# Optimization experiments

Measured on AMD Instinct MI355X. Metric: run time of the kernel, lower is better.

## Reference

```python
import jax, jax.numpy as jnp
import numpy as np

EMBED_DIM = 768
NUM_HEADS = 12
FF_DIM = 3072
HEAD_DIM = EMBED_DIM // NUM_HEADS
LN_EPS = 1e-5


def setup_inputs() -> dict:
    key = jax.random.key(0)
    ks = jax.random.split(key, 10)
    C, F = EMBED_DIM, FF_DIM
    s = lambda d: 1.0 / np.sqrt(d)
    return {
        "x": jax.random.normal(ks[0], (2, 2048, C), dtype=jnp.float32),
        "w_qkv": jax.random.normal(ks[1], (C, 3 * C), dtype=jnp.float32) * s(C),
        "w_out": jax.random.normal(ks[2], (C, C), dtype=jnp.float32) * s(C),
        "ln1_g": jnp.ones((C,), jnp.float32),
        "ln1_b": jnp.zeros((C,), jnp.float32),
        "ln2_g": jnp.ones((C,), jnp.float32),
        "ln2_b": jnp.zeros((C,), jnp.float32),
        "w1": jax.random.normal(ks[3], (C, F), dtype=jnp.float32) * s(C),
        "b1": jnp.zeros((F,), jnp.float32),
        "w2": jax.random.normal(ks[4], (F, C), dtype=jnp.float32) * s(F),
        "b2": jnp.zeros((C,), jnp.float32),
    }


def _layernorm(x, g, b):
    mu = jnp.mean(x, axis=-1, keepdims=True)
    var = jnp.var(x, axis=-1, keepdims=True)
    return (x - mu) * jax.lax.rsqrt(var + LN_EPS) * g + b


def _attention(x, w_qkv, w_out):
    B, T, C = x.shape
    qkv = x @ w_qkv                               # [B,T,3C]
    q, k, v = jnp.split(qkv, 3, axis=2)
    def heads(t):  # [B,T,C] -> [B,H,T,Dh]
        return t.reshape(B, T, NUM_HEADS, HEAD_DIM).transpose(0, 2, 1, 3)
    q, k, v = heads(q), heads(k), heads(v)
    att = jnp.einsum("bhqd,bhkd->bhqk", q, k) / np.sqrt(HEAD_DIM)
    mask = jnp.tril(jnp.ones((T, T), bool))
    att = jnp.where(mask, att, -jnp.inf)
    att = jax.nn.softmax(att, axis=-1)
    out = jnp.einsum("bhqk,bhkd->bhqd", att, v)   # [B,H,T,Dh]
    out = out.transpose(0, 2, 1, 3).reshape(B, T, C)
    return out @ w_out


def reference(x, w_qkv, w_out, ln1_g, ln1_b, ln2_g, ln2_b, w1, b1, w2, b2):
    x = x + _attention(_layernorm(x, ln1_g, ln1_b), w_qkv, w_out)
    h = _layernorm(x, ln2_g, ln2_b)
    h = jax.nn.gelu(h @ w1 + b1, approximate=False) @ w2 + b2
    return x + h
```

## Files before the change

### kernel.cpp

```cpp
#include <hip/hip_runtime.h>
#include <hip/hip_bf16.h>
#include <math.h>

typedef __attribute__((ext_vector_type(8))) short short8;
typedef __attribute__((ext_vector_type(4))) float f32x4;
typedef __attribute__((address_space(1))) const void CG;
typedef __attribute__((address_space(3))) void LS;

#define LOAD_LDS16(src, dst) __builtin_amdgcn_global_load_lds((CG*)(src), (LS*)(dst), 16, 0, 0)

__device__ __forceinline__ short f2bf(float f) {
  union { float f; unsigned u; } v; v.f = f;
  unsigned r = v.u + 0x7fffu + ((v.u >> 16) & 1u);
  return (short)(r >> 16);
}

__global__ __launch_bounds__(256) void transp_all(const float* __restrict__ w_qkv,
                                                  const float* __restrict__ w_out,
                                                  const float* __restrict__ w1,
                                                  const float* __restrict__ w2,
                                                  short* __restrict__ wqkvT,
                                                  short* __restrict__ woutT,
                                                  short* __restrict__ w1T,
                                                  short* __restrict__ w2T) {
  __shared__ short t[32][33];
  int bid = blockIdx.x;
  const float* W; short* Wt; int K, N, nx, id;
  if (bid < 1728)      { W = w_qkv; Wt = wqkvT; K = 768;  N = 2304; nx = 72; id = bid; }
  else if (bid < 2304) { W = w_out; Wt = woutT; K = 768;  N = 768;  nx = 24; id = bid - 1728; }
  else if (bid < 4608) { W = w1;    Wt = w1T;   K = 768;  N = 3072; nx = 96; id = bid - 2304; }
  else                 { W = w2;    Wt = w2T;   K = 3072; N = 768;  nx = 24; id = bid - 4608; }
  int n0 = (id % nx) << 5, k0 = (id / nx) << 5;
  int tid = threadIdx.x;
#pragma unroll
  for (int p = 0; p < 4; ++p) {
    int e = tid + (p << 8);
    int r = e >> 5, c = e & 31;
    t[r][c] = f2bf(W[(size_t)(k0 + r) * N + n0 + c]);
  }
  __syncthreads();
#pragma unroll
  for (int p = 0; p < 4; ++p) {
    int e = tid + (p << 8);
    int r = e >> 5, c = e & 31;
    Wt[(size_t)(n0 + r) * K + k0 + c] = t[c][r];
  }
}

__global__ __launch_bounds__(256) void ln_kernel(const float* __restrict__ x,
                                                 const float* __restrict__ g,
                                                 const float* __restrict__ b,
                                                 short* __restrict__ out) {
  int row = blockIdx.x;
  const float* xr = x + (size_t)row * 768;
  int tid = threadIdx.x;
  float v0 = xr[tid], v1 = xr[tid + 256], v2 = xr[tid + 512];
  float s = v0 + v1 + v2;
  float ss = v0 * v0 + v1 * v1 + v2 * v2;
#pragma unroll
  for (int m = 1; m < 64; m <<= 1) { s += __shfl_xor(s, m); ss += __shfl_xor(ss, m); }
  __shared__ float red[8];
  int w = tid >> 6;
  if ((tid & 63) == 0) { red[w] = s; red[w + 4] = ss; }
  __syncthreads();
  s = red[0] + red[1] + red[2] + red[3];
  ss = red[4] + red[5] + red[6] + red[7];
  float mean = s * (1.0f / 768.0f);
  float var = ss * (1.0f / 768.0f) - mean * mean;
  float rs = rsqrtf(var + 1e-5f);
  short* outr = out + (size_t)row * 768;
  outr[tid]       = f2bf((v0 - mean) * rs * g[tid]       + b[tid]);
  outr[tid + 256] = f2bf((v1 - mean) * rs * g[tid + 256] + b[tid + 256]);
  outr[tid + 512] = f2bf((v2 - mean) * rs * g[tid + 512] + b[tid + 512]);
}

template <int EPI>
__global__ __launch_bounds__(512, 4) void gemm512(
    const short* __restrict__ A, const short* __restrict__ Bt,
    int M, int N, int K,
    short* __restrict__ outQ, short* __restrict__ outK, short* __restrict__ outVt,
    float* __restrict__ outF, short* __restrict__ outB,
    const float* __restrict__ bias, const float* __restrict__ resid) {
  __shared__ short lA[2][128 * 32];
  __shared__ short lB[2][256 * 32];
  int tid = threadIdx.x;
  int lane = tid & 63, w = tid >> 6;
  int li = lane & 15, g = lane >> 4;
  int wr = w >> 2, wc = w & 3;

  int nx = gridDim.x, ny = gridDim.y;
  int nwg = nx * ny;
  int fid = (int)blockIdx.y * nx + (int)blockIdx.x;
  int nid = (fid & 7) * (nwg >> 3) + (fid >> 3);
  const int GM = 8;
  int npg = GM * nx;
  int grp = nid / npg;
  int fm = grp * GM;
  int gs = min(GM, ny - fm);
  int lid = nid - grp * npg;
  int bm = (fm + lid % gs) << 7;
  int bn = (lid / gs) << 8;

  size_t lda = (EPI == 4) ? 3072 : (size_t)K;
  int koff = (EPI == 4) ? (int)blockIdx.z * 1536 : 0;

  int lr = lane >> 2;
  int lcs = (lane & 3) ^ ((lr ^ (lr >> 2)) & 3);
  const short* aSrc  = A + (size_t)(bm + w * 16 + lr) * lda + koff + lcs * 8;
  const short* bSrc0 = Bt + (size_t)(bn + w * 32 + lr) * lda + koff + lcs * 8;
  const short* bSrc1 = Bt + (size_t)(bn + w * 32 + 16 + lr) * lda + koff + lcs * 8;

#define STG(buf, ki)                                                  \
  do {                                                                \
    int kk = (ki) << 5;                                               \
    LOAD_LDS16(aSrc + kk, (char*)lA[buf] + (w << 10));                \
    LOAD_LDS16(bSrc0 + kk, (char*)lB[buf] + (w << 11));               \
    LOAD_LDS16(bSrc1 + kk, (char*)lB[buf] + (w << 11) + 1024);        \
  } while (0)

  f32x4 zero = {0.f, 0.f, 0.f, 0.f};
  f32x4 acc[4][4];
#pragma unroll
  for (int i = 0; i < 4; ++i)
#pragma unroll
    for (int j = 0; j < 4; ++j) acc[i][j] = zero;

  int sg = (g ^ ((li ^ (li >> 2)) & 3)) << 3;

  int nk = K >> 5;
  STG(0, 0);
  for (int ki = 0; ki < nk; ++ki) {
    int cur = ki & 1;
    __syncthreads();
    if (ki + 1 < nk) STG(cur ^ 1, ki + 1);
    const short* Ac = lA[cur];
    const short* Bc = lB[cur];
    short8 af[4], bf[4];
#pragma unroll
    for (int rt = 0; rt < 4; ++rt)
      af[rt] = *(const short8*)&Ac[(wr * 64 + rt * 16 + li) * 32 + sg];
#pragma unroll
    for (int ct = 0; ct < 4; ++ct)
      bf[ct] = *(const short8*)&Bc[(wc * 64 + ct * 16 + li) * 32 + sg];
#pragma unroll
    for (int rt = 0; rt < 4; ++rt)
#pragma unroll
      for (int ct = 0; ct < 4; ++ct)
        acc[rt][ct] = __builtin_amdgcn_mfma_f32_16x16x32_bf16(af[rt], bf[ct], acc[rt][ct], 0, 0, 0);
  }
#undef STG

#pragma unroll
  for (int rt = 0; rt < 4; ++rt) {
    int mbase = bm + wr * 64 + rt * 16 + g * 4;
#pragma unroll
    for (int ct = 0; ct < 4; ++ct) {
      int n = bn + wc * 64 + ct * 16 + li;
      f32x4 c = acc[rt][ct];
      if (EPI == 0) {
        if (n < 768) {
          int h = n >> 6, d = n & 63;
#pragma unroll
          for (int i = 0; i < 4; ++i) {
            int tok = mbase + i;
            int bb = tok >> 11, t = tok & 2047;
            outQ[((size_t)((bb * 12 + h) * 2048 + t) << 6) + d] = f2bf(c[i]);
          }
        } else if (n < 1536) {
          int nn = n - 768;
          int h = nn >> 6, d = nn & 63;
#pragma unroll
          for (int i = 0; i < 4; ++i) {
            int tok = mbase + i;
            int bb = tok >> 11, t = tok & 2047;
            outK[((size_t)((bb * 12 + h) * 2048 + t) << 6) + d] = f2bf(c[i]);
          }
        } else {
          int nn = n - 1536;
          int h = nn >> 6, d = nn & 63;
          int bb = mbase >> 11, t = mbase & 2047;
          ushort4 pk;
          pk.x = (unsigned short)f2bf(c[0]);
          pk.y = (unsigned short)f2bf(c[1]);
          pk.z = (unsigned short)f2bf(c[2]);
          pk.w = (unsigned short)f2bf(c[3]);
          *(ushort4*)((unsigned short*)outVt + (((size_t)((bb * 12 + h) * 64 + d)) << 11) + t) = pk;
        }
      } else if (EPI == 1) {
#pragma unroll
        for (int i = 0; i < 4; ++i) {
          int m = mbase + i;
          outF[(size_t)m * N + n] = c[i] + resid[(size_t)m * N + n];
        }
      } else if (EPI == 2) {
        float bv = bias[n];
#pragma unroll
        for (int i = 0; i < 4; ++i) {
          int m = mbase + i;
          float xx = c[i] + bv;
          float gel = 0.5f * xx * (1.0f + erff(xx * 0.70710678118654752f));
          outB[(size_t)m * N + n] = f2bf(gel);
        }
      } else {
        bool last = (blockIdx.z == 1);
        float bv = last ? bias[n] : 0.f;
#pragma unroll
        for (int i = 0; i < 4; ++i) {
          int m = mbase + i;
          float add = c[i] + bv + (last ? resid[(size_t)m * N + n] : 0.f);
          atomicAdd(&outF[(size_t)m * N + n], add);
        }
      }
    }
  }
}

__global__ __launch_bounds__(256, 3) void attn_kernel(const short* __restrict__ Q,
                                                      const short* __restrict__ Kk,
                                                      const short* __restrict__ Vt,
                                                      unsigned short* __restrict__ o_part,
                                                      float* __restrict__ ml_part) {
  __shared__ short lK[2][64 * 64];
  __shared__ short lV[2][64 * 64];
  __shared__ short lP[4][32 * 64];
  int tid = threadIdx.x;
  int lane = tid & 63, w = tid >> 6;
  int li = lane & 15, g = lane >> 4;
  int bh = blockIdx.y;
  int cid = 39 - (int)blockIdx.x;
  int qt = 0, cum = 0;
  while (true) { int n = (qt >> 2) + 1; if (cid < cum + n) break; cum += n; ++qt; }
  int c = cid - cum;
  int nch = (qt >> 2) + 1;
  int nt = (qt + 1) << 1;
  int bq = nt / nch, rem = nt % nch;
  int t0 = c * bq + (c < rem ? c : rem);
  int t1 = t0 + bq + (c < rem ? 1 : 0);

  int qbase = (qt << 7) + (w << 5);
  const short* Qb = Q + ((size_t)bh << 17);
  const short* Kb = Kk + ((size_t)bh << 17);
  const short* Vb = Vt + ((size_t)bh << 17);

  short8 qf[2][2];
#pragma unroll
  for (int rt = 0; rt < 2; ++rt)
#pragma unroll
    for (int kc = 0; kc < 2; ++kc)
      qf[rt][kc] = *(const short8*)&Qb[(size_t)(qbase + rt * 16 + li) * 64 + kc * 32 + g * 8];

  int r0 = tid >> 3, s0 = (tid & 7) ^ (r0 & 7);
  int r1 = r0 + 32,  s1 = (tid & 7) ^ (r1 & 7);
  const short* kS0 = Kb + r0 * 64 + s0 * 8;
  const short* kS1 = Kb + r1 * 64 + s1 * 8;
  const short* vS0 = Vb + (size_t)r0 * 2048 + s0 * 8;
  const short* vS1 = Vb + (size_t)r1 * 2048 + s1 * 8;

#define STAGE(buf, kt)                                                        \
  do {                                                                        \
    LOAD_LDS16(kS0 + (size_t)(kt) * 4096, (char*)lK[buf] + (w << 10));        \
    LOAD_LDS16(kS1 + (size_t)(kt) * 4096, (char*)lK[buf] + 4096 + (w << 10)); \
    LOAD_LDS16(vS0 + (size_t)(kt) * 64,   (char*)lV[buf] + (w << 10));        \
    LOAD_LDS16(vS1 + (size_t)(kt) * 64,   (char*)lV[buf] + 4096 + (w << 10)); \
  } while (0)

  const short8 kOnes = {0x3F80, 0x3F80, 0x3F80, 0x3F80, 0x3F80, 0x3F80, 0x3F80, 0x3F80};
  f32x4 zero = {0.f, 0.f, 0.f, 0.f};
  f32x4 o[2][4];
  f32x4 lrow[2];
  float mrow[2] = {-1e30f, -1e30f};
#pragma unroll
  for (int rt = 0; rt < 2; ++rt) {
    lrow[rt] = zero;
#pragma unroll
    for (int ct = 0; ct < 4; ++ct) o[rt][ct] = zero;
  }

  int diagKt = qbase >> 6;
  const float SCALE = 0.18033688011112042f;
  int sw = li & 7;
  unsigned short* Pw = (unsigned short*)lP[w];

  STAGE(0, t0);

  for (int kt = t0; kt < t1; ++kt) {
    int cur = (kt - t0) & 1;
    __syncthreads();
    if (kt + 1 < t1) STAGE(cur ^ 1, kt + 1);

    if (kt <= diagKt) {
      const short* Kc = lK[cur];
      const short* Vc = lV[cur];

      f32x4 s[2][4];
#pragma unroll
      for (int rt = 0; rt < 2; ++rt)
#pragma unroll
        for (int ct = 0; ct < 4; ++ct) s[rt][ct] = zero;
#pragma unroll
      for (int kc = 0; kc < 2; ++kc)
#pragma unroll
        for (int ct = 0; ct < 4; ++ct) {
          short8 kf = *(const short8*)&Kc[(ct * 16 + li) * 64 + ((((kc << 2) | g) ^ sw) << 3)];
#pragma unroll
          for (int rt = 0; rt < 2; ++rt)
            s[rt][ct] = __builtin_amdgcn_mfma_f32_16x16x32_bf16(qf[rt][kc], kf, s[rt][ct], 0, 0, 0);
        }

      if (kt == diagKt) {
        int kb0 = kt << 6;
#pragma unroll
        for (int rt = 0; rt < 2; ++rt) {
          int qrow0 = qbase + rt * 16 + g * 4;
#pragma unroll
          for (int ct = 0; ct < 4; ++ct) {
            int kcol = kb0 + ct * 16 + li;
#pragma unroll
            for (int i = 0; i < 4; ++i)
              if (kcol > qrow0 + i) s[rt][ct][i] = -1e30f;
          }
        }
      }

#pragma unroll
      for (int rt = 0; rt < 2; ++rt) {
        float tm = s[rt][0][0];
#pragma unroll
        for (int ct = 0; ct < 4; ++ct)
#pragma unroll
          for (int i = 0; i < 4; ++i) tm = fmaxf(tm, s[rt][ct][i]);
#pragma unroll
        for (int m2 = 1; m2 < 64; m2 <<= 1) tm = fmaxf(tm, __shfl_xor(tm, m2));
        if (tm > mrow[rt] + 8.0f) {
          float corr = exp2f((mrow[rt] - tm) * SCALE);
          mrow[rt] = tm;
#pragma unroll
          for (int i = 0; i < 4; ++i) lrow[rt][i] *= corr;
#pragma unroll
          for (int ct = 0; ct < 4; ++ct)
#pragma unroll
            for (int i = 0; i < 4; ++i) o[rt][ct][i] *= corr;
        }
#pragma unroll
        for (int ct = 0; ct < 4; ++ct)
#pragma unroll
          for (int i = 0; i < 4; ++i) {
            float p = exp2f((s[rt][ct][i] - mrow[rt]) * SCALE);
            int row = rt * 16 + (g << 2) + i;
            int col = (ct << 4) + li;
            int ch = (col >> 3) ^ (row & 7);
            Pw[(row << 6) + (ch << 3) + (col & 7)] = (unsigned short)f2bf(p);
          }
      }

      f32x4 psum[2];
      psum[0] = zero; psum[1] = zero;
#pragma unroll
      for (int kc = 0; kc < 2; ++kc) {
        short8 vf[4];
#pragma unroll
        for (int ct = 0; ct < 4; ++ct)
          vf[ct] = *(const short8*)&Vc[(ct * 16 + li) * 64 + ((((kc << 2) | g) ^ sw) << 3)];
#pragma unroll
        for (int rt = 0; rt < 2; ++rt) {
          short8 pf = *(const short8*)&lP[w][(rt * 16 + li) * 64 + ((((kc << 2) | g) ^ sw) << 3)];
#pragma unroll
          for (int ct = 0; ct < 4; ++ct)
            o[rt][ct] = __builtin_amdgcn_mfma_f32_16x16x32_bf16(pf, vf[ct], o[rt][ct], 0, 0, 0);
          psum[rt] = __builtin_amdgcn_mfma_f32_16x16x32_bf16(pf, kOnes, psum[rt], 0, 0, 0);
        }
      }
#pragma unroll
      for (int rt = 0; rt < 2; ++rt)
#pragma unroll
        for (int i = 0; i < 4; ++i) lrow[rt][i] += psum[rt][i];
    }
  }
#undef STAGE

  int pid = bh * 40 + cid;
#pragma unroll
  for (int rt = 0; rt < 2; ++rt)
#pragma unroll
    for (int ct = 0; ct < 4; ++ct) {
      int col = (ct << 4) + li;
      int row0 = (w << 5) + (rt << 4) + (g << 2);
      ushort4 pk;
      pk.x = (unsigned short)f2bf(o[rt][ct][0]);
      pk.y = (unsigned short)f2bf(o[rt][ct][1]);
      pk.z = (unsigned short)f2bf(o[rt][ct][2]);
      pk.w = (unsigned short)f2bf(o[rt][ct][3]);
      *(ushort4*)&o_part[((size_t)pid * 64 + col) * 128 + row0] = pk;
    }
  if (li == 0) {
    float2* mlp = (float2*)ml_part;
#pragma unroll
    for (int rt = 0; rt < 2; ++rt)
#pragma unroll
      for (int i = 0; i < 4; ++i) {
        int row = (w << 5) + (rt << 4) + (g << 2) + i;
        mlp[(size_t)pid * 128 + row] = make_float2(mrow[rt], lrow[rt][i]);
      }
  }
}

__global__ __launch_bounds__(256) void attn_combine(const unsigned short* __restrict__ o_part,
                                                    const float* __restrict__ ml_part,
                                                    short* __restrict__ O) {
  __shared__ float wgt[4][128];
  int qt = blockIdx.x, bh = blockIdx.y;
  int a = qt >> 2, bb = qt & 3;
  int c0 = 2 * a * (a - 1) + a * bb + qt;
  int nch = a + 1;
  int pid0 = bh * 40 + c0;
  int tid = threadIdx.x;
  const float SCALE = 0.18033688011112042f;
  const float2* mlp = (const float2*)ml_part;

  if (tid < 128) {
    int row = tid;
    float mv[4] = {-1e30f, -1e30f, -1e30f, -1e30f};
    float lv[4] = {0.f, 0.f, 0.f, 0.f};
#pragma unroll
    for (int c = 0; c < 4; ++c)
      if (c < nch) {
        float2 ml = mlp[(size_t)(pid0 + c) * 128 + row];
        mv[c] = ml.x; lv[c] = ml.y;
      }
    float M = fmaxf(fmaxf(mv[0], mv[1]), fmaxf(mv[2], mv[3]));
    float u[4];
    float L = 0.f;
#pragma unroll
    for (int c = 0; c < 4; ++c) {
      u[c] = (c < nch) ? exp2f((mv[c] - M) * SCALE) : 0.f;
      L += lv[c] * u[c];
    }
    float inv = 1.0f / L;
#pragma unroll
    for (int c = 0; c < 4; ++c) wgt[c][row] = u[c] * inv;
  }
  __syncthreads();

  int col = tid & 63, rg = tid >> 6;
  int b = bh / 12, h = bh % 12;
  size_t obase[4];
#pragma unroll
  for (int c = 0; c < 4; ++c) obase[c] = ((size_t)(pid0 + c) * 64 + col) * 128;
  for (int r = 0; r < 32; ++r) {
    int row = (rg << 5) + r;
    float acc = 0.f;
#pragma unroll
    for (int c = 0; c < 4; ++c)
      if (c < nch) {
        union { unsigned u; float f; } cv;
        cv.u = ((unsigned)o_part[obase[c] + row]) << 16;
        acc += cv.f * wgt[c][row];
      }
    int t = (qt << 7) + row;
    O[((size_t)(b * 2048 + t)) * 768 + h * 64 + col] = f2bf(acc);
  }
}

extern "C" void kernel_launch(void* const* d_in, const int* in_sizes, int n_in,
                              void* d_out, int out_size, void* d_ws, size_t ws_size,
                              hipStream_t stream) {
  const float* x     = (const float*)d_in[0];
  const float* w_qkv = (const float*)d_in[1];
  const float* w_out = (const float*)d_in[2];
  const float* ln1g  = (const float*)d_in[3];
  const float* ln1b  = (const float*)d_in[4];
  const float* ln2g  = (const float*)d_in[5];
  const float* ln2b  = (const float*)d_in[6];
  const float* w1    = (const float*)d_in[7];
  const float* b1    = (const float*)d_in[8];
  const float* w2    = (const float*)d_in[9];
  const float* b2    = (const float*)d_in[10];
  float* out = (float*)d_out;
  char* ws = (char*)d_ws;

  short* wqkvT = (short*)(ws + 0);
  short* woutT = (short*)(ws + 3538944);
  short* w1T   = (short*)(ws + 4718592);
  short* w2T   = (short*)(ws + 9437184);
  short* qb    = (short*)(ws + 14155776);
  short* kb    = (short*)(ws + 20447232);
  short* vtb   = (short*)(ws + 26738688);
  short* attnb = (short*)(ws + 33030144);
  short* ab    = qb;
  short* xnb   = (short*)(ws + 39321600);
  float* x2b   = (float*)(ws + 45613056);
  unsigned short* o_part = (unsigned short*)(ws + 39321600);
  float* ml_part = (float*)(ws + 55050240);

  transp_all<<<dim3(6912), 256, 0, stream>>>(w_qkv, w_out, w1, w2, wqkvT, woutT, w1T, w2T);

  ln_kernel<<<dim3(4096), 256, 0, stream>>>(x, ln1g, ln1b, xnb);

  gemm512<0><<<dim3(9, 32), 512, 0, stream>>>(xnb, wqkvT, 4096, 2304, 768,
                                              qb, kb, vtb, nullptr, nullptr, nullptr, nullptr);

  attn_kernel<<<dim3(40, 24), 256, 0, stream>>>(qb, kb, vtb, o_part, ml_part);
  attn_combine<<<dim3(16, 24), 256, 0, stream>>>(o_part, ml_part, attnb);

  gemm512<1><<<dim3(3, 32), 512, 0, stream>>>(attnb, woutT, 4096, 768, 768,
                                              nullptr, nullptr, nullptr, x2b, nullptr, nullptr, x);

  ln_kernel<<<dim3(4096), 256, 0, stream>>>(x2b, ln2g, ln2b, xnb);

  gemm512<2><<<dim3(12, 32), 512, 0, stream>>>(xnb, w1T, 4096, 3072, 768,
                                               nullptr, nullptr, nullptr, nullptr, ab, b1, nullptr);

  hipMemsetAsync(out, 0, (size_t)4096 * 768 * 4, stream);
  gemm512<4><<<dim3(3, 32, 2), 512, 0, stream>>>(ab, w2T, 4096, 768, 1536,
                                                 nullptr, nullptr, nullptr, out, nullptr, b2, x2b);
}
```

Baseline: 263.4 us.

## Add 256x256x64 eight-phase pipelined GEMM for QKV, FFN1 and FFN2

New measurement: 288.3 us. +9.4%, slower.

```diff
diff --git a/kernel.cpp b/kernel.cpp
--- a/kernel.cpp
+++ b/kernel.cpp
@@ -75,6 +75,201 @@
 }
 
 template <int EPI>
+__global__ __launch_bounds__(512, 2) void gemm8p(
+    const short* __restrict__ A, const short* __restrict__ Bt,
+    int M, int N, int K,
+    short* __restrict__ outQ, short* __restrict__ outK, short* __restrict__ outVt,
+    float* __restrict__ outF, short* __restrict__ outB,
+    const float* __restrict__ bias, const float* __restrict__ resid) {
+  __shared__ short lA[2][256 * 64];
+  __shared__ short lB[2][256 * 64];
+  int tid = threadIdx.x;
+  int lane = tid & 63, w = tid >> 6;
+  int li = lane & 15, g = lane >> 4;
+  int wr = w >> 2, wc = w & 3;
+
+  int nx = gridDim.x, ny = gridDim.y;
+  int nwg = nx * ny;
+  int fid = (int)blockIdx.y * nx + (int)blockIdx.x;
+  int q8 = nwg >> 3, r8 = nwg & 7;
+  int xcd = fid & 7, idx = fid >> 3;
+  int nid = (xcd < r8 ? xcd * (q8 + 1) : r8 * (q8 + 1) + (xcd - r8) * q8) + idx;
+  const int GM = 8;
+  int npg = GM * nx;
+  int grp = nid / npg;
+  int fm = grp * GM;
+  int gs = min(GM, ny - fm);
+  int lid = nid - grp * npg;
+  int bm = (fm + lid % gs) << 8;
+  int bn = (lid / gs) << 8;
+
+  size_t lda = (EPI == 4) ? 3072 : (size_t)K;
+  int koff = (EPI == 4) ? (int)blockIdx.z * 768 : 0;
+  int Keff = (EPI == 4) ? 768 : K;
+
+  int baseRow = (w << 3) + (lane >> 3);
+  int csrc = (lane & 7) ^ (lane >> 3);
+  const short* aS = A + (size_t)(bm + baseRow) * lda + koff + csrc * 8;
+  const short* bS = Bt + (size_t)(bn + baseRow) * lda + koff + csrc * 8;
+
+#define STG_HALF(buf, h, kk)                                                              \
+  do {                                                                                    \
+    if ((h) < 2) {                                                                        \
+      LOAD_LDS16(aS + (size_t)((h) * 128) * lda + (kk),      (char*)lA[buf] + (h) * 16384 + (w << 10)); \
+      LOAD_LDS16(aS + (size_t)((h) * 128 + 64) * lda + (kk), (char*)lA[buf] + (h) * 16384 + 8192 + (w << 10)); \
+    } else {                                                                              \
+      LOAD_LDS16(bS + (size_t)(((h) - 2) * 128) * lda + (kk),      (char*)lB[buf] + ((h) - 2) * 16384 + (w << 10)); \
+      LOAD_LDS16(bS + (size_t)(((h) - 2) * 128 + 64) * lda + (kk), (char*)lB[buf] + ((h) - 2) * 16384 + 8192 + (w << 10)); \
+    }                                                                                     \
+  } while (0)
+
+  f32x4 zero = {0.f, 0.f, 0.f, 0.f};
+  f32x4 acc[8][4];
+#pragma unroll
+  for (int i = 0; i < 8; ++i)
+#pragma unroll
+    for (int j = 0; j < 4; ++j) acc[i][j] = zero;
+
+  short8 afr[4][2], bfr[2][2];
+
+#define RD_A(Lc, rh)                                                                      \
+  _Pragma("unroll") for (int rt = 0; rt < 4; ++rt)                                        \
+  _Pragma("unroll") for (int kc = 0; kc < 2; ++kc)                                        \
+    afr[rt][kc] = *(const short8*)&(Lc)[(wr * 128 + (rh) * 64 + rt * 16 + li) * 64 + ((((kc << 2) | g) ^ (li & 7)) << 3)];
+
+#define RD_B(Lc, chh)                                                                     \
+  _Pragma("unroll") for (int ct = 0; ct < 2; ++ct)                                        \
+  _Pragma("unroll") for (int kc = 0; kc < 2; ++kc)                                        \
+    bfr[ct][kc] = *(const short8*)&(Lc)[(wc * 64 + (chh) * 32 + ct * 16 + li) * 64 + ((((kc << 2) | g) ^ (li & 7)) << 3)];
+
+#define MF(rh, chh)                                                                       \
+  __builtin_amdgcn_s_setprio(1);                                                          \
+  _Pragma("unroll") for (int rt = 0; rt < 4; ++rt)                                        \
+  _Pragma("unroll") for (int ct = 0; ct < 2; ++ct)                                        \
+  _Pragma("unroll") for (int kc = 0; kc < 2; ++kc)                                        \
+    acc[(rh) * 4 + rt][(chh) * 2 + ct] = __builtin_amdgcn_mfma_f32_16x16x32_bf16(         \
+        afr[rt][kc], bfr[ct][kc], acc[(rh) * 4 + rt][(chh) * 2 + ct], 0, 0, 0);           \
+  __builtin_amdgcn_s_setprio(0);
+
+#define SB __builtin_amdgcn_sched_barrier(0)
+#define LGKM0 asm volatile("s_waitcnt lgkmcnt(0)" ::: "memory")
+
+  int nk = Keff >> 6;
+  STG_HALF(0, 0, 0); STG_HALF(0, 1, 0); STG_HALF(0, 2, 0); STG_HALF(0, 3, 0);
+
+  for (int t = 0; t < nk; ++t) {
+    int c = t & 1, nb = c ^ 1;
+    int kk1 = (t + 1) << 6;
+    bool pf = (t + 1 < nk);
+    const short* Ac = lA[c];
+    const short* Bc = lB[c];
+    if (pf) {
+      STG_HALF(nb, 0, kk1);
+      SB;
+      asm volatile("s_waitcnt vmcnt(2)" ::: "memory");
+    } else {
+      asm volatile("s_waitcnt vmcnt(0)" ::: "memory");
+    }
+    SB;
+    __builtin_amdgcn_s_barrier();
+    SB;
+    RD_A(Ac, 0);
+    RD_B(Bc, 0);
+    LGKM0; SB;
+    MF(0, 0);
+    SB;
+    if (pf) STG_HALF(nb, 1, kk1);
+    SB;
+    __builtin_amdgcn_s_barrier();
+    SB;
+    RD_B(Bc, 1);
+    LGKM0; SB;
+    MF(0, 1);
+    SB;
+    if (pf) STG_HALF(nb, 2, kk1);
+    SB;
+    __builtin_amdgcn_s_barrier();
+    SB;
+    RD_A(Ac, 1);
+    LGKM0; SB;
+    MF(1, 1);
+    SB;
+    if (pf) STG_HALF(nb, 3, kk1);
+    SB;
+    __builtin_amdgcn_s_barrier();
+    SB;
+    RD_B(Bc, 0);
+    LGKM0; SB;
+    MF(1, 0);
+    SB;
+  }
+#undef STG_HALF
+#undef RD_A
+#undef RD_B
+#undef MF
+#undef SB
+#undef LGKM0
+
+#pragma unroll
+  for (int rt = 0; rt < 8; ++rt) {
+    int mbase = bm + wr * 128 + rt * 16 + g * 4;
+#pragma unroll
+    for (int ct = 0; ct < 4; ++ct) {
+      int n = bn + wc * 64 + ct * 16 + li;
+      f32x4 cvv = acc[rt][ct];
+      if (EPI == 0) {
+        if (n < 768) {
+          int h = n >> 6, d = n & 63;
+#pragma unroll
+          for (int i = 0; i < 4; ++i) {
+            int tok = mbase + i;
+            int bb = tok >> 11, tt = tok & 2047;
+            outQ[((size_t)((bb * 12 + h) * 2048 + tt) << 6) + d] = f2bf(cvv[i]);
+          }
+        } else if (n < 1536) {
+          int nn = n - 768;
+          int h = nn >> 6, d = nn & 63;
+#pragma unroll
+          for (int i = 0; i < 4; ++i) {
+            int tok = mbase + i;
+            int bb = tok >> 11, tt = tok & 2047;
+            outK[((size_t)((bb * 12 + h) * 2048 + tt) << 6) + d] = f2bf(cvv[i]);
+          }
+        } else {
+          int nn = n - 1536;
+          int h = nn >> 6, d = nn & 63;
+          int bb = mbase >> 11, tt = mbase & 2047;
+          ushort4 pk;
+          pk.x = (unsigned short)f2bf(cvv[0]);
+          pk.y = (unsigned short)f2bf(cvv[1]);
+          pk.z = (unsigned short)f2bf(cvv[2]);
+          pk.w = (unsigned short)f2bf(cvv[3]);
+          *(ushort4*)((unsigned short*)outVt + (((size_t)((bb * 12 + h) * 64 + d)) << 11) + tt) = pk;
+        }
+      } else if (EPI == 2) {
+        float bv = bias[n];
+#pragma unroll
+        for (int i = 0; i < 4; ++i) {
+          int m = mbase + i;
+          float xx = cvv[i] + bv;
+          float gel = 0.5f * xx * (1.0f + erff(xx * 0.70710678118654752f));
+          outB[(size_t)m * N + n] = f2bf(gel);
+        }
+      } else {
+        bool last = (blockIdx.z == 3);
+        float bv = last ? bias[n] : 0.f;
+#pragma unroll
+        for (int i = 0; i < 4; ++i) {
+          int m = mbase + i;
+          float add = cvv[i] + bv + (last ? resid[(size_t)m * N + n] : 0.f);
+          atomicAdd(&outF[(size_t)m * N + n], add);
+        }
+      }
+    }
+  }
+}
+
+template <int EPI>
 __global__ __launch_bounds__(512, 4) void gemm512(
     const short* __restrict__ A, const short* __restrict__ Bt,
     int M, int N, int K,
@@ -101,14 +296,13 @@
   int bm = (fm + lid % gs) << 7;
   int bn = (lid / gs) << 8;
 
-  size_t lda = (EPI == 4) ? 3072 : (size_t)K;
-  int koff = (EPI == 4) ? (int)blockIdx.z * 1536 : 0;
+  size_t lda = (size_t)K;
 
   int lr = lane >> 2;
   int lcs = (lane & 3) ^ ((lr ^ (lr >> 2)) & 3);
-  const short* aSrc  = A + (size_t)(bm + w * 16 + lr) * lda + koff + lcs * 8;
-  const short* bSrc0 = Bt + (size_t)(bn + w * 32 + lr) * lda + koff + lcs * 8;
-  const short* bSrc1 = Bt + (size_t)(bn + w * 32 + 16 + lr) * lda + koff + lcs * 8;
+  const short* aSrc  = A + (size_t)(bm + w * 16 + lr) * lda + lcs * 8;
+  const short* bSrc0 = Bt + (size_t)(bn + w * 32 + lr) * lda + lcs * 8;
+  const short* bSrc1 = Bt + (size_t)(bn + w * 32 + 16 + lr) * lda + lcs * 8;
 
 #define STG(buf, ki)                                                  \
   do {                                                                \
@@ -157,58 +351,11 @@
     for (int ct = 0; ct < 4; ++ct) {
       int n = bn + wc * 64 + ct * 16 + li;
       f32x4 c = acc[rt][ct];
-      if (EPI == 0) {
-        if (n < 768) {
-          int h = n >> 6, d = n & 63;
-#pragma unroll
-          for (int i = 0; i < 4; ++i) {
-            int tok = mbase + i;
-            int bb = tok >> 11, t = tok & 2047;
-            outQ[((size_t)((bb * 12 + h) * 2048 + t) << 6) + d] = f2bf(c[i]);
-          }
-        } else if (n < 1536) {
-          int nn = n - 768;
-          int h = nn >> 6, d = nn & 63;
-#pragma unroll
-          for (int i = 0; i < 4; ++i) {
-            int tok = mbase + i;
-            int bb = tok >> 11, t = tok & 2047;
-            outK[((size_t)((bb * 12 + h) * 2048 + t) << 6) + d] = f2bf(c[i]);
-          }
-        } else {
-          int nn = n - 1536;
-          int h = nn >> 6, d = nn & 63;
-          int bb = mbase >> 11, t = mbase & 2047;
-          ushort4 pk;
-          pk.x = (unsigned short)f2bf(c[0]);
-          pk.y = (unsigned short)f2bf(c[1]);
-          pk.z = (unsigned short)f2bf(c[2]);
-          pk.w = (unsigned short)f2bf(c[3]);
-          *(ushort4*)((unsigned short*)outVt + (((size_t)((bb * 12 + h) * 64 + d)) << 11) + t) = pk;
-        }
-      } else if (EPI == 1) {
+      if (EPI == 1) {
 #pragma unroll
         for (int i = 0; i < 4; ++i) {
           int m = mbase + i;
           outF[(size_t)m * N + n] = c[i] + resid[(size_t)m * N + n];
-        }
-      } else if (EPI == 2) {
-        float bv = bias[n];
-#pragma unroll
-        for (int i = 0; i < 4; ++i) {
-          int m = mbase + i;
-          float xx = c[i] + bv;
-          float gel = 0.5f * xx * (1.0f + erff(xx * 0.70710678118654752f));
-          outB[(size_t)m * N + n] = f2bf(gel);
-        }
-      } else {
-        bool last = (blockIdx.z == 1);
-        float bv = last ? bias[n] : 0.f;
-#pragma unroll
-        for (int i = 0; i < 4; ++i) {
-          int m = mbase + i;
-          float add = c[i] + bv + (last ? resid[(size_t)m * N + n] : 0.f);
-          atomicAdd(&outF[(size_t)m * N + n], add);
         }
       }
     }
@@ -496,8 +643,8 @@
 
   ln_kernel<<<dim3(4096), 256, 0, stream>>>(x, ln1g, ln1b, xnb);
 
-  gemm512<0><<<dim3(9, 32), 512, 0, stream>>>(xnb, wqkvT, 4096, 2304, 768,
-                                              qb, kb, vtb, nullptr, nullptr, nullptr, nullptr);
+  gemm8p<0><<<dim3(9, 16), 512, 0, stream>>>(xnb, wqkvT, 4096, 2304, 768,
+                                             qb, kb, vtb, nullptr, nullptr, nullptr, nullptr);
 
   attn_kernel<<<dim3(40, 24), 256, 0, stream>>>(qb, kb, vtb, o_part, ml_part);
   attn_combine<<<dim3(16, 24), 256, 0, stream>>>(o_part, ml_part, attnb);
@@ -507,10 +654,10 @@
 
   ln_kernel<<<dim3(4096), 256, 0, stream>>>(x2b, ln2g, ln2b, xnb);
 
-  gemm512<2><<<dim3(12, 32), 512, 0, stream>>>(xnb, w1T, 4096, 3072, 768,
-                                               nullptr, nullptr, nullptr, nullptr, ab, b1, nullptr);
+  gemm8p<2><<<dim3(12, 16), 512, 0, stream>>>(xnb, w1T, 4096, 3072, 768,
+                                              nullptr, nullptr, nullptr, nullptr, ab, b1, nullptr);
 
   hipMemsetAsync(out, 0, (size_t)4096 * 768 * 4, stream);
-  gemm512<4><<<dim3(3, 32, 2), 512, 0, stream>>>(ab, w2T, 4096, 768, 1536,
-                                                 nullptr, nullptr, nullptr, out, nullptr, b2, x2b);
-}
+  gemm8p<4><<<dim3(3, 16, 4), 512, 0, stream>>>(ab, w2T, 4096, 768, 768,
+                                                nullptr, nullptr, nullptr, out, nullptr, b2, x2b);
+}
```

## Retile GEMMs to 128x128x64 with 256 threads and split-K of four

Applied to the files above, without the earlier changes.

New measurement: 271.4 us. +3.0%, slower.

```diff
diff --git a/kernel.cpp b/kernel.cpp
--- a/kernel.cpp
+++ b/kernel.cpp
@@ -75,23 +75,25 @@
 }
 
 template <int EPI>
-__global__ __launch_bounds__(512, 4) void gemm512(
+__global__ __launch_bounds__(256, 2) void gemm64(
     const short* __restrict__ A, const short* __restrict__ Bt,
     int M, int N, int K,
     short* __restrict__ outQ, short* __restrict__ outK, short* __restrict__ outVt,
     float* __restrict__ outF, short* __restrict__ outB,
     const float* __restrict__ bias, const float* __restrict__ resid) {
-  __shared__ short lA[2][128 * 32];
-  __shared__ short lB[2][256 * 32];
+  __shared__ short lA[2][128 * 64];
+  __shared__ short lB[2][128 * 64];
   int tid = threadIdx.x;
   int lane = tid & 63, w = tid >> 6;
   int li = lane & 15, g = lane >> 4;
-  int wr = w >> 2, wc = w & 3;
+  int wrow = (w >> 1) << 6, wcol = (w & 1) << 6;
 
   int nx = gridDim.x, ny = gridDim.y;
   int nwg = nx * ny;
   int fid = (int)blockIdx.y * nx + (int)blockIdx.x;
-  int nid = (fid & 7) * (nwg >> 3) + (fid >> 3);
+  int q8 = nwg >> 3, rr8 = nwg & 7;
+  int xcd = fid & 7, idx = fid >> 3;
+  int nid = (xcd < rr8 ? xcd * (q8 + 1) : rr8 * (q8 + 1) + (xcd - rr8) * q8) + idx;
   const int GM = 8;
   int npg = GM * nx;
   int grp = nid / npg;
@@ -99,23 +101,26 @@
   int gs = min(GM, ny - fm);
   int lid = nid - grp * npg;
   int bm = (fm + lid % gs) << 7;
-  int bn = (lid / gs) << 8;
+  int bn = (lid / gs) << 7;
 
   size_t lda = (EPI == 4) ? 3072 : (size_t)K;
-  int koff = (EPI == 4) ? (int)blockIdx.z * 1536 : 0;
-
-  int lr = lane >> 2;
-  int lcs = (lane & 3) ^ ((lr ^ (lr >> 2)) & 3);
-  const short* aSrc  = A + (size_t)(bm + w * 16 + lr) * lda + koff + lcs * 8;
-  const short* bSrc0 = Bt + (size_t)(bn + w * 32 + lr) * lda + koff + lcs * 8;
-  const short* bSrc1 = Bt + (size_t)(bn + w * 32 + 16 + lr) * lda + koff + lcs * 8;
-
-#define STG(buf, ki)                                                  \
-  do {                                                                \
-    int kk = (ki) << 5;                                               \
-    LOAD_LDS16(aSrc + kk, (char*)lA[buf] + (w << 10));                \
-    LOAD_LDS16(bSrc0 + kk, (char*)lB[buf] + (w << 11));               \
-    LOAD_LDS16(bSrc1 + kk, (char*)lB[buf] + (w << 11) + 1024);        \
+  int koff = (EPI == 4) ? (int)blockIdx.z * 768 : 0;
+  int Keff = (EPI == 4) ? 768 : K;
+
+  int r8 = tid >> 3;
+  int csrc = (tid & 7) ^ (r8 & 7);
+  const short* aS = A + (size_t)(bm + r8) * lda + koff + csrc * 8;
+  const short* bS = Bt + (size_t)(bn + r8) * lda + koff + csrc * 8;
+
+#define STG(buf, ki)                                                                  \
+  do {                                                                                \
+    int kk = (ki) << 6;                                                               \
+    _Pragma("unroll") for (int p = 0; p < 4; ++p) {                                   \
+      LOAD_LDS16(aS + (size_t)(p * 32) * lda + kk,                                    \
+                 (char*)lA[buf] + (p * 32 + w * 8) * 128);                            \
+      LOAD_LDS16(bS + (size_t)(p * 32) * lda + kk,                                    \
+                 (char*)lB[buf] + (p * 32 + w * 8) * 128);                            \
+    }                                                                                 \
   } while (0)
 
   f32x4 zero = {0.f, 0.f, 0.f, 0.f};
@@ -125,9 +130,8 @@
 #pragma unroll
     for (int j = 0; j < 4; ++j) acc[i][j] = zero;
 
-  int sg = (g ^ ((li ^ (li >> 2)) & 3)) << 3;
-
-  int nk = K >> 5;
+  int sw7 = li & 7;
+  int nk = Keff >> 6;
   STG(0, 0);
   for (int ki = 0; ki < nk; ++ki) {
     int cur = ki & 1;
@@ -135,27 +139,33 @@
     if (ki + 1 < nk) STG(cur ^ 1, ki + 1);
     const short* Ac = lA[cur];
     const short* Bc = lB[cur];
-    short8 af[4], bf[4];
+    short8 af[4][2], bf[4][2];
 #pragma unroll
     for (int rt = 0; rt < 4; ++rt)
-      af[rt] = *(const short8*)&Ac[(wr * 64 + rt * 16 + li) * 32 + sg];
+#pragma unroll
+      for (int kc = 0; kc < 2; ++kc)
+        af[rt][kc] = *(const short8*)&Ac[(wrow + rt * 16 + li) * 64 + ((((kc << 2) | g) ^ sw7) << 3)];
 #pragma unroll
     for (int ct = 0; ct < 4; ++ct)
-      bf[ct] = *(const short8*)&Bc[(wc * 64 + ct * 16 + li) * 32 + sg];
+#pragma unroll
+      for (int kc = 0; kc < 2; ++kc)
+        bf[ct][kc] = *(const short8*)&Bc[(wcol + ct * 16 + li) * 64 + ((((kc << 2) | g) ^ sw7) << 3)];
 #pragma unroll
     for (int rt = 0; rt < 4; ++rt)
 #pragma unroll
       for (int ct = 0; ct < 4; ++ct)
-        acc[rt][ct] = __builtin_amdgcn_mfma_f32_16x16x32_bf16(af[rt], bf[ct], acc[rt][ct], 0, 0, 0);
+#pragma unroll
+        for (int kc = 0; kc < 2; ++kc)
+          acc[rt][ct] = __builtin_amdgcn_mfma_f32_16x16x32_bf16(af[rt][kc], bf[ct][kc], acc[rt][ct], 0, 0, 0);
   }
 #undef STG
 
 #pragma unroll
   for (int rt = 0; rt < 4; ++rt) {
-    int mbase = bm + wr * 64 + rt * 16 + g * 4;
+    int mbase = bm + wrow + rt * 16 + g * 4;
 #pragma unroll
     for (int ct = 0; ct < 4; ++ct) {
-      int n = bn + wc * 64 + ct * 16 + li;
+      int n = bn + wcol + ct * 16 + li;
       f32x4 c = acc[rt][ct];
       if (EPI == 0) {
         if (n < 768) {
@@ -202,7 +212,7 @@
           outB[(size_t)m * N + n] = f2bf(gel);
         }
       } else {
-        bool last = (blockIdx.z == 1);
+        bool last = (blockIdx.z == 3);
         float bv = last ? bias[n] : 0.f;
 #pragma unroll
         for (int i = 0; i < 4; ++i) {
@@ -496,21 +506,21 @@
 
   ln_kernel<<<dim3(4096), 256, 0, stream>>>(x, ln1g, ln1b, xnb);
 
-  gemm512<0><<<dim3(9, 32), 512, 0, stream>>>(xnb, wqkvT, 4096, 2304, 768,
+  gemm64<0><<<dim3(18, 32), 256, 0, stream>>>(xnb, wqkvT, 4096, 2304, 768,
                                               qb, kb, vtb, nullptr, nullptr, nullptr, nullptr);
 
   attn_kernel<<<dim3(40, 24), 256, 0, stream>>>(qb, kb, vtb, o_part, ml_part);
   attn_combine<<<dim3(16, 24), 256, 0, stream>>>(o_part, ml_part, attnb);
 
-  gemm512<1><<<dim3(3, 32), 512, 0, stream>>>(attnb, woutT, 4096, 768, 768,
-                                              nullptr, nullptr, nullptr, x2b, nullptr, nullptr, x);
+  gemm64<1><<<dim3(6, 32), 256, 0, stream>>>(attnb, woutT, 4096, 768, 768,
+                                             nullptr, nullptr, nullptr, x2b, nullptr, nullptr, x);
 
   ln_kernel<<<dim3(4096), 256, 0, stream>>>(x2b, ln2g, ln2b, xnb);
 
-  gemm512<2><<<dim3(12, 32), 512, 0, stream>>>(xnb, w1T, 4096, 3072, 768,
-                                               nullptr, nullptr, nullptr, nullptr, ab, b1, nullptr);
+  gemm64<2><<<dim3(24, 32), 256, 0, stream>>>(xnb, w1T, 4096, 3072, 768,
+                                              nullptr, nullptr, nullptr, nullptr, ab, b1, nullptr);
 
   hipMemsetAsync(out, 0, (size_t)4096 * 768 * 4, stream);
-  gemm512<4><<<dim3(3, 32, 2), 512, 0, stream>>>(ab, w2T, 4096, 768, 1536,
-                                                 nullptr, nullptr, nullptr, out, nullptr, b2, x2b);
-}
+  gemm64<4><<<dim3(6, 32, 4), 256, 0, stream>>>(ab, w2T, 4096, 768, 768,
+                                                nullptr, nullptr, nullptr, out, nullptr, b2, x2b);
+}
```
